# Kernel tuning notes

Measured on AMD Instinct MI355X. Metric: run time of the kernel, lower is better.

Reference implementation:

```python
import jax, jax.numpy as jnp
import numpy as np
from math import comb

FILTER_SIZE = 4
UP = 2


def _make_kernel(filter_size=FILTER_SIZE):
    # binomial filter, outer product, normalized to sum 1 (matches torch buffer)
    f = np.array([comb(filter_size - 1, j) for j in range(filter_size)], dtype=np.float32)
    k = np.outer(f, f)
    k /= k.sum()
    return jnp.asarray(k)


def setup_inputs() -> dict:
    key = jax.random.key(0)
    x = jax.random.normal(key, (8, 128, 128, 128), dtype=jnp.float32)  # [B,C,H,W]
    kernel = _make_kernel()  # [4,4], sums to 1
    return {"x": x, "kernel": kernel}


def reference(x, kernel):
    # upfirdn2d.upsample2d(x, kernel, up=2):
    #   zero-insert upsample by 2, pad ((k+up-1)//2, (k-up)//2), FIR filter with gain=up^2.
    B, C, H, W = x.shape
    kh, kw = kernel.shape
    gain = UP * UP
    f = (kernel * gain)[::-1, ::-1]  # flip for correlation-vs-conv (symmetric kernel: no-op)
    pad0 = (kh + UP - 1) // 2          # = 2 for k=4, up=2
    pad1 = (kh - UP) // 2              # = 1
    # lhs_dilation gives size up*H-(up-1); zero-insertion gives up*H (trailing zeros),
    # so add (up-1) extra padding on the high side.
    pad_lo, pad_hi = pad0, pad1 + (UP - 1)
    w = jnp.broadcast_to(f, (C, 1, kh, kw))  # depthwise filter, same blur per channel
    out = jax.lax.conv_general_dilated(
        x, w,
        window_strides=(1, 1),
        padding=((pad_lo, pad_hi), (pad_lo, pad_hi)),
        lhs_dilation=(UP, UP),
        dimension_numbers=("NCHW", "OIHW", "NCHW"),
        feature_group_count=C,
    )  # [B, C, 2H, 2W]
    return out
```

## Files before the change

### kernel.cpp

```cpp
#include <hip/hip_runtime.h>


__global__ __launch_bounds__(256) void Upsample_63797444215162_kernel(
    const float* __restrict__ x, float* __restrict__ out)
{
    const int tid = blockIdx.x * 256 + threadIdx.x;
    const int t   = tid & 31;
    const int y   = (tid >> 5) & 255;
    const int bc  = tid >> 13;

    const int yi  = y >> 1;
    const int odd = y & 1;
    const int   rA = odd ? yi     : yi - 1;
    const int   rB = odd ? yi + 1 : yi;
    const float wA = odd ? 0.75f : 0.25f;
    const float wB = odd ? 0.25f : 0.75f;

    const float* base = x + (size_t)bc * (128 * 128);
    const int c0 = t << 2;

    float e0 = 0.f, e1 = 0.f, e2 = 0.f, e3 = 0.f, e4 = 0.f, e5 = 0.f;

    if (rA >= 0) {
        const float* r = base + rA * 128 + c0;
        const float4 v = *(const float4*)r;
        e1 = wA * v.x; e2 = wA * v.y; e3 = wA * v.z; e4 = wA * v.w;
        if (c0 > 0)       e0 = wA * r[-1];
        if (c0 + 4 < 128) e5 = wA * r[4];
    }
    if (rB < 128) {
        const float* r = base + rB * 128 + c0;
        const float4 v = *(const float4*)r;
        e1 += wB * v.x; e2 += wB * v.y; e3 += wB * v.z; e4 += wB * v.w;
        if (c0 > 0)       e0 += wB * r[-1];
        if (c0 + 4 < 128) e5 += wB * r[4];
    }

    float4 o0, o1;
    o0.x = 0.25f * e0 + 0.75f * e1;
    o0.y = 0.75f * e1 + 0.25f * e2;
    o0.z = 0.25f * e1 + 0.75f * e2;
    o0.w = 0.75f * e2 + 0.25f * e3;
    o1.x = 0.25f * e2 + 0.75f * e3;
    o1.y = 0.75f * e3 + 0.25f * e4;
    o1.z = 0.25f * e3 + 0.75f * e4;
    o1.w = 0.75f * e4 + 0.25f * e5;

    float* op = out + ((size_t)(bc * 256 + y) * 256 + (t << 3));
    *(float4*)op       = o0;
    *((float4*)op + 1) = o1;
}

extern "C" void kernel_launch(void* const* d_in, const int* in_sizes, int n_in,
                              void* d_out, int out_size, void* d_ws, size_t ws_size,
                              hipStream_t stream) {
    const float* x = (const float*)d_in[0];
    float* out = (float*)d_out;
    Upsample_63797444215162_kernel<<<32768, 256, 0, stream>>>(x, out);
}
```

Before: 331.8 us.

## Compute both output rows per input row and share horizontal halo via wave shuffles

```diff
diff --git a/kernel.cpp b/kernel.cpp
--- a/kernel.cpp
+++ b/kernel.cpp
@@ -5,50 +5,44 @@
     const float* __restrict__ x, float* __restrict__ out)
 {
     const int tid = blockIdx.x * 256 + threadIdx.x;
-    const int t   = tid & 31;
-    const int y   = (tid >> 5) & 255;
-    const int bc  = tid >> 13;
+    const int c  = tid & 63;
+    const int m  = (tid >> 6) & 127;
+    const int bc = tid >> 13;
 
-    const int yi  = y >> 1;
-    const int odd = y & 1;
-    const int   rA = odd ? yi     : yi - 1;
-    const int   rB = odd ? yi + 1 : yi;
-    const float wA = odd ? 0.75f : 0.25f;
-    const float wB = odd ? 0.25f : 0.75f;
+    const float* plane = x + (size_t)bc * (128 * 128);
+    const float* row0  = plane + m * 128 + (c << 1);
 
-    const float* base = x + (size_t)bc * (128 * 128);
-    const int c0 = t << 2;
+    float2 vm1 = make_float2(0.f, 0.f);
+    float2 vp1 = make_float2(0.f, 0.f);
+    const float2 v0 = *(const float2*)row0;
+    if (m > 0)   vm1 = *(const float2*)(row0 - 128);
+    if (m < 127) vp1 = *(const float2*)(row0 + 128);
 
-    float e0 = 0.f, e1 = 0.f, e2 = 0.f, e3 = 0.f, e4 = 0.f, e5 = 0.f;
+    const float e0 = 0.25f * vm1.x + 0.75f * v0.x;
+    const float e1 = 0.25f * vm1.y + 0.75f * v0.y;
+    const float q0 = 0.75f * v0.x + 0.25f * vp1.x;
+    const float q1 = 0.75f * v0.y + 0.25f * vp1.y;
 
-    if (rA >= 0) {
-        const float* r = base + rA * 128 + c0;
-        const float4 v = *(const float4*)r;
-        e1 = wA * v.x; e2 = wA * v.y; e3 = wA * v.z; e4 = wA * v.w;
-        if (c0 > 0)       e0 = wA * r[-1];
-        if (c0 + 4 < 128) e5 = wA * r[4];
-    }
-    if (rB < 128) {
-        const float* r = base + rB * 128 + c0;
-        const float4 v = *(const float4*)r;
-        e1 += wB * v.x; e2 += wB * v.y; e3 += wB * v.z; e4 += wB * v.w;
-        if (c0 > 0)       e0 += wB * r[-1];
-        if (c0 + 4 < 128) e5 += wB * r[4];
-    }
+    float eL = __shfl_up(e1, 1);
+    float eR = __shfl_down(e0, 1);
+    float qL = __shfl_up(q1, 1);
+    float qR = __shfl_down(q0, 1);
+    if (c == 0)  { eL = 0.f; qL = 0.f; }
+    if (c == 63) { eR = 0.f; qR = 0.f; }
 
-    float4 o0, o1;
-    o0.x = 0.25f * e0 + 0.75f * e1;
-    o0.y = 0.75f * e1 + 0.25f * e2;
-    o0.z = 0.25f * e1 + 0.75f * e2;
-    o0.w = 0.75f * e2 + 0.25f * e3;
-    o1.x = 0.25f * e2 + 0.75f * e3;
-    o1.y = 0.75f * e3 + 0.25f * e4;
-    o1.z = 0.25f * e3 + 0.75f * e4;
-    o1.w = 0.75f * e4 + 0.25f * e5;
+    float4 re, ro;
+    re.x = 0.25f * eL + 0.75f * e0;
+    re.y = 0.75f * e0 + 0.25f * e1;
+    re.z = 0.25f * e0 + 0.75f * e1;
+    re.w = 0.75f * e1 + 0.25f * eR;
+    ro.x = 0.25f * qL + 0.75f * q0;
+    ro.y = 0.75f * q0 + 0.25f * q1;
+    ro.z = 0.25f * q0 + 0.75f * q1;
+    ro.w = 0.75f * q1 + 0.25f * qR;
 
-    float* op = out + ((size_t)(bc * 256 + y) * 256 + (t << 3));
-    *(float4*)op       = o0;
-    *((float4*)op + 1) = o1;
+    float* op = out + ((size_t)(bc * 256 + (m << 1)) * 256 + (c << 2));
+    *(float4*)op         = re;
+    *(float4*)(op + 256) = ro;
 }
 
 extern "C" void kernel_launch(void* const* d_in, const int* in_sizes, int n_in,
```

After: 305.1 us. 1.09x faster.
